# Performance work log

Measured on AMD Instinct MI355X. Metric: run time of the kernel, lower is better.

## Reference

```python
import jax, jax.numpy as jnp
import numpy as np

B, N, DIM, HEADS = 8, 512, 512, 16
MAX_DIST, NG = 128, 32
RBF_STOP = 20.0
EPS = 1e-5


def _ln(x, g, b):
    m = jnp.mean(x, axis=-1, keepdims=True)
    v = jnp.mean((x - m) ** 2, axis=-1, keepdims=True)
    return (x - m) * jax.lax.rsqrt(v + EPS) * g + b


def setup_inputs() -> dict:
    key = jax.random.key(0)
    ks = jax.random.split(key, 12)
    d = DIM
    s = 0.02
    return {
        "x": jax.random.normal(ks[0], (B * N, d), jnp.float32),
        "dist_matrix": jax.random.randint(ks[1], (B, N, N), 0, MAX_DIST, jnp.int32),
        "dist_3d": jax.random.uniform(ks[2], (B, N, N), jnp.float32) * RBF_STOP,
        "norm1_g": jnp.ones((d,), jnp.float32),
        "norm1_b": jnp.zeros((d,), jnp.float32),
        "in_proj_w": jax.random.normal(ks[3], (3 * d, d), jnp.float32) * s,
        "in_proj_b": jnp.zeros((3 * d,), jnp.float32),
        "out_proj_w": jax.random.normal(ks[4], (d, d), jnp.float32) * s,
        "out_proj_b": jnp.zeros((d,), jnp.float32),
        "dist_emb": jax.random.normal(ks[5], (MAX_DIST, HEADS), jnp.float32) * s,
        "rbf_w": jax.random.normal(ks[6], (HEADS, NG), jnp.float32) * s,
        "rbf_b": jnp.zeros((HEADS,), jnp.float32),
        "norm2_g": jnp.ones((d,), jnp.float32),
        "norm2_b": jnp.zeros((d,), jnp.float32),
        "ffn_w1": jax.random.normal(ks[7], (4 * d, d), jnp.float32) * s,
        "ffn_b1": jnp.zeros((4 * d,), jnp.float32),
        "ffn_w2": jax.random.normal(ks[8], (d, 4 * d), jnp.float32) * s,
        "ffn_b2": jnp.zeros((d,), jnp.float32),
        "batch": jnp.repeat(jnp.arange(B, dtype=jnp.int32), N),
    }


def reference(x, dist_matrix, dist_3d, norm1_g, norm1_b, in_proj_w, in_proj_b,
              out_proj_w, out_proj_b, dist_emb, rbf_w, rbf_b, norm2_g, norm2_b,
              ffn_w1, ffn_b1, ffn_w2, ffn_b2, batch):
    b, n = dist_matrix.shape[0], dist_matrix.shape[1]
    d = x.shape[-1]
    dh = d // HEADS
    # equal-size graphs -> to_dense_batch is a reshape, mask all-true
    xd = x.reshape(b, n, d)

    # additive attention bias: shortest-path-distance embedding + RBF projection
    dc = jnp.clip(dist_matrix, 0, MAX_DIST - 1)
    bias_spd = dist_emb[dc]                                  # [b, n, n, H]
    offset = jnp.linspace(0.0, RBF_STOP, NG, dtype=jnp.float32)
    coeff = -0.5 / (RBF_STOP / (NG - 1)) ** 2
    rbf = jnp.exp(coeff * (dist_3d[..., None] - offset) ** 2)  # [b, n, n, NG]
    bias_3d = rbf @ rbf_w.T + rbf_b                          # [b, n, n, H]
    bias = jnp.transpose(bias_spd + bias_3d, (0, 3, 1, 2))   # [b, H, n, n]

    # multi-head attention (pre-norm residual, as in source)
    h = _ln(xd, norm1_g, norm1_b)
    qkv = h @ in_proj_w.T + in_proj_b
    q, k, v = jnp.split(qkv, 3, axis=-1)
    q = q.reshape(b, n, HEADS, dh).transpose(0, 2, 1, 3)
    k = k.reshape(b, n, HEADS, dh).transpose(0, 2, 1, 3)
    v = v.reshape(b, n, HEADS, dh).transpose(0, 2, 1, 3)
    scores = jnp.einsum('bhqd,bhkd->bhqk', q, k) / jnp.sqrt(jnp.float32(dh)) + bias
    attn = jax.nn.softmax(scores, axis=-1)
    ctx = jnp.einsum('bhqk,bhkd->bhqd', attn, v)
    ctx = ctx.transpose(0, 2, 1, 3).reshape(b, n, d)
    attn_out = ctx @ out_proj_w.T + out_proj_b
    h = h + attn_out

    # FFN (dropout inactive at eval)
    h2 = _ln(h, norm2_g, norm2_b)
    ff = jax.nn.gelu(h2 @ ffn_w1.T + ffn_b1, approximate=False) @ ffn_w2.T + ffn_b2
    h = h + ff
    return h.reshape(b * n, d)
```

## Files before the change

### kernel.cpp

```cpp
#include <hip/hip_runtime.h>
#include <hip/hip_bf16.h>
#include <math.h>

#define BB 8
#define NN 512
#define DD 512
#define NH 16
#define DH 32
#define TD 1536
#define NG 32
#define MAXD 128

typedef __attribute__((ext_vector_type(8))) short bf16x8;
typedef __attribute__((ext_vector_type(4))) float f32x4;
typedef __attribute__((ext_vector_type(2))) unsigned int u32x2;
typedef __attribute__((ext_vector_type(4))) unsigned int u32x4;

__device__ inline short f2bf(float x) {
    __hip_bfloat16 h = __float2bfloat16(x);
    return *reinterpret_cast<short*>(&h);
}
__device__ inline float bf2f(short x) {
    union { unsigned u; float f; } c;
    c.u = ((unsigned)(unsigned short)x) << 16;
    return c.f;
}
__device__ inline unsigned cvt_pk_bf16(float lo, float hi) {
    unsigned r;
    asm("v_cvt_pk_bf16_f32 %0, %1, %2" : "=v"(r) : "v"(lo), "v"(hi));
    return r;
}
__device__ inline float exp2fast(float x) {
    float r;
    asm("v_exp_f32 %0, %1" : "=v"(r) : "v"(x));
    return r;
}

__device__ inline void gld_lds16(const void* g, void* l) {
    __builtin_amdgcn_global_load_lds(
        (const __attribute__((address_space(1))) unsigned int*)g,
        (__attribute__((address_space(3))) unsigned int*)l, 16, 0, 0);
}

__global__ __launch_bounds__(256) void cvt_weights(
    const float* __restrict__ s0, const float* __restrict__ s1,
    const float* __restrict__ s2, const float* __restrict__ s3,
    short* __restrict__ d0, short* __restrict__ d1,
    short* __restrict__ d2, short* __restrict__ d3,
    const float* __restrict__ rbfw, const float* __restrict__ rbfb,
    short* __restrict__ Tg,
    int n0, int n1, int n2, int n3) {
    if (blockIdx.y == 4) {
        if (blockIdx.x != 0) return;
        const float STEP  = 20.0f / 31.0f;
        const float COEFF = -0.5f / (STEP * STEP);
        for (int idx = threadIdx.x; idx < 194 * 16; idx += 256) {
            const int i = idx >> 4, h = idx & 15;
            const float x = fminf((float)i, 192.0f) * (20.0f / 192.0f);
            float acc = rbfb[h];
#pragma unroll
            for (int g = 0; g < NG; g++) {
                const float t = x - (float)g * STEP;
                acc += __expf(COEFF * t * t) * rbfw[h * NG + g];
            }
            Tg[idx] = f2bf(acc * 1.44269504088896f);
        }
        return;
    }
    const float* s; short* d; int n;
    switch (blockIdx.y) {
        case 0: s = s0; d = d0; n = n0; break;
        case 1: s = s1; d = d1; n = n1; break;
        case 2: s = s2; d = d2; n = n2; break;
        default: s = s3; d = d3; n = n3; break;
    }
    const int i = (blockIdx.x * 256 + threadIdx.x) * 4;
    if (i >= n) return;
    const float4 v = *(const float4*)(s + i);
    short4 o;
    o.x = f2bf(v.x); o.y = f2bf(v.y); o.z = f2bf(v.z); o.w = f2bf(v.w);
    *(short4*)(d + i) = o;
}

__global__ __launch_bounds__(256) void ln_kernel(const float* __restrict__ x,
                                                 const float* __restrict__ g,
                                                 const float* __restrict__ b,
                                                 short* __restrict__ out_bf) {
    const int row = blockIdx.x;
    const int tid = threadIdx.x;
    const int wave = tid >> 6, lane = tid & 63;
    const float* xr = x + (size_t)row * DD;
    const float v0 = xr[tid], v1 = xr[tid + 256];
    float s = v0 + v1, q = v0 * v0 + v1 * v1;
#pragma unroll
    for (int m = 1; m < 64; m <<= 1) { s += __shfl_xor(s, m); q += __shfl_xor(q, m); }
    __shared__ float ps[8];
    if (lane == 0) { ps[wave] = s; ps[wave + 4] = q; }
    __syncthreads();
    s = ps[0] + ps[1] + ps[2] + ps[3];
    q = ps[4] + ps[5] + ps[6] + ps[7];
    const float mean = s * (1.0f / DD);
    const float var  = q * (1.0f / DD) - mean * mean;
    const float rs   = rsqrtf(var + 1e-5f);
    out_bf[(size_t)row * DD + tid]       = f2bf((v0 - mean) * rs * g[tid] + b[tid]);
    out_bf[(size_t)row * DD + tid + 256] = f2bf((v1 - mean) * rs * g[tid + 256] + b[tid + 256]);
}

template <int TM, bool GELU, int RESMODE, bool OUTBF>
__global__ __launch_bounds__(256) void gemm_bf16(
    const short* __restrict__ A, const short* __restrict__ Bw,
    const float* __restrict__ bias, const void* __restrict__ res,
    void* __restrict__ Cout, int M, int Nout, int K) {
    const int MI = TM / 32;
    const int bm = blockIdx.y * TM;
    const int bn = blockIdx.x * 128;
    const int tid  = threadIdx.x;
    const int wave = tid >> 6;
    const int lane = tid & 63;
    const int l16  = lane & 15;
    const int quad = lane >> 4;
    const int wr = (wave >> 1) * (TM / 2);
    const int wc = (wave & 1) * 64;

    __shared__ short As[2][TM * 32];
    __shared__ short Bs[2][128 * 32];

    f32x4 acc[MI][4];
#pragma unroll
    for (int i = 0; i < MI; i++)
#pragma unroll
        for (int j = 0; j < 4; j++) acc[i][j] = (f32x4){0.f, 0.f, 0.f, 0.f};

    auto stage = [&](int buf, int k0) {
        const short* Ab = A + (size_t)bm * K + k0;
        const short* Bb = Bw + (size_t)bn * K + k0;
#pragma unroll
        for (int j = 0; j < TM / 64; j++) {
            const int idx = j * 256 + wave * 64 + lane;
            gld_lds16(Ab + (size_t)(idx >> 2) * K + (idx & 3) * 8,
                      &As[buf][(size_t)(j * 256 + wave * 64) * 8]);
        }
#pragma unroll
        for (int j = 0; j < 2; j++) {
            const int idx = j * 256 + wave * 64 + lane;
            gld_lds16(Bb + (size_t)(idx >> 2) * K + (idx & 3) * 8,
                      &Bs[buf][(size_t)(j * 256 + wave * 64) * 8]);
        }
    };
    auto compute = [&](int buf) {
        bf16x8 af[MI], bfr[4];
#pragma unroll
        for (int i = 0; i < MI; i++)
            af[i] = *(const bf16x8*)&As[buf][(wr + i * 16 + l16) * 32 + quad * 8];
#pragma unroll
        for (int j = 0; j < 4; j++)
            bfr[j] = *(const bf16x8*)&Bs[buf][(wc + j * 16 + l16) * 32 + quad * 8];
#pragma unroll
        for (int i = 0; i < MI; i++)
#pragma unroll
            for (int j = 0; j < 4; j++)
                acc[i][j] = __builtin_amdgcn_mfma_f32_16x16x32_bf16(af[i], bfr[j], acc[i][j], 0, 0, 0);
    };

    stage(0, 0);
    __syncthreads();
    int cur = 0;
    for (int k0 = 32; k0 < K; k0 += 32) {
        stage(cur ^ 1, k0);
        compute(cur);
        __syncthreads();
        cur ^= 1;
    }
    compute(cur);

#pragma unroll
    for (int i = 0; i < MI; i++) {
#pragma unroll
        for (int r = 0; r < 4; r++) {
            const int row = bm + wr + i * 16 + quad * 4 + r;
#pragma unroll
            for (int j = 0; j < 4; j++) {
                const int col = bn + wc + j * 16 + l16;
                float v = acc[i][j][r] + bias[col];
                if (GELU) v = 0.5f * v * (1.0f + erff(v * 0.70710678118654752f));
                if (RESMODE == 1) v += ((const float*)res)[(size_t)row * Nout + col];
                if (RESMODE == 2) v += bf2f(((const short*)res)[(size_t)row * Nout + col]);
                if (OUTBF) ((short*)Cout)[(size_t)row * Nout + col] = f2bf(v);
                else       ((float*)Cout)[(size_t)row * Nout + col] = v;
            }
        }
    }
}

__global__ __launch_bounds__(512, 2) void attn_mfma(
    const short* __restrict__ qkv,
    const int* __restrict__ dist,
    const float* __restrict__ dist3d,
    const float* __restrict__ demb,
    const short* __restrict__ Tg,
    short* __restrict__ Obf) {
    const int blk  = blockIdx.x;
    const int b    = blk & 7;
    const int q0   = (blk >> 3) * 16;
    const int tid  = threadIdx.x;
    const int wave = tid >> 6;
    const int lane = tid & 63;
    const int l16  = lane & 15;
    const int quad = lane >> 4;
    const int hh0  = wave * 2;

    __shared__ short Vc[2][NH * 1024];
    __shared__ short Pb[16 * 512];
    __shared__ short Tt[194 * 18];
    __shared__ short Db[128 * 18];
    __shared__ unsigned short Pk[512 * 16];

    for (int i = tid; i < 194 * 16; i += 512) Tt[(i >> 4) * 18 + (i & 15)] = Tg[i];
    for (int i = tid; i < 128 * 16; i += 512)
        Db[(i >> 4) * 18 + (i & 15)] = f2bf(demb[i] * 1.44269504088896f);
    {
        const size_t rb = ((size_t)(b * NN) + q0) * NN;
#pragma unroll
        for (int q = 0; q < 16; q++) {
            const size_t off = rb + (size_t)q * NN + tid;
            int dc = dist[off];
            dc = min(max(dc, 0), MAXD - 1);
            int ii = (int)(dist3d[off] * 9.6f + 0.5f);
            ii = min(ii, 192);
            Pk[tid * 16 + q] = (unsigned short)(dc | (ii << 8));
        }
    }

    const float scale = 0.17677669529663687f * 1.44269504088896f;
    bf16x8 qf[2];
#pragma unroll
    for (int h = 0; h < 2; h++)
        qf[h] = *(const bf16x8*)(qkv + (size_t)(b * NN + q0 + l16) * TD + (hh0 + h) * DH + quad * 8);

    f32x4 O[2][2];
    float lsum[2][4];
#pragma unroll
    for (int h = 0; h < 2; h++) {
#pragma unroll
        for (int tt = 0; tt < 2; tt++) O[h][tt] = (f32x4){0.f, 0.f, 0.f, 0.f};
#pragma unroll
        for (int r = 0; r < 4; r++) lsum[h][r] = 0.f;
    }

    __syncthreads();

    const int sk = lane >> 2;
    const int sc = lane & 3;

    auto stageV = [&](int buf, int c) {
        const size_t rowb = (size_t)(b * NN + c * 32 + sk) * TD + 2 * DD + sc * 8;
#pragma unroll
        for (int h = 0; h < 2; h++) {
            short* dst = &Vc[buf][(hh0 + h) * 1024];
            gld_lds16(qkv + rowb + (hh0 + h) * DH, dst);
            gld_lds16(qkv + rowb + (size_t)16 * TD + (hh0 + h) * DH, dst + 512);
        }
    };
    auto loadK = [&](int c, bf16x8 (*kd)[2]) {
#pragma unroll
        for (int h = 0; h < 2; h++) {
            const short* base =
                qkv + (size_t)(b * NN + c * 32 + l16) * TD + DD + (hh0 + h) * DH + quad * 8;
            kd[h][0] = *(const bf16x8*)base;
            kd[h][1] = *(const bf16x8*)(base + 16 * TD);
        }
    };

    bf16x8 kf[2][2], kfn[2][2];
    stageV(0, 0);
    loadK(0, kf);
    int cur = 0;

    for (int c = 0; c < 16; c++) {
        asm volatile("" ::: "memory");
        __builtin_amdgcn_s_waitcnt(0x0F70);
        asm volatile("" ::: "memory");

        u32x2 vraw[2][4];
#pragma unroll
        for (int h = 0; h < 2; h++) {
            const unsigned va =
                (unsigned)(uintptr_t)&Vc[cur][(hh0 + h) * 1024 + quad * 128 + l16];
            asm volatile("ds_read_b64_tr_b16 %0, %1 offset:0"    : "=v"(vraw[h][0]) : "v"(va));
            asm volatile("ds_read_b64_tr_b16 %0, %1 offset:128"  : "=v"(vraw[h][1]) : "v"(va));
            asm volatile("ds_read_b64_tr_b16 %0, %1 offset:1024" : "=v"(vraw[h][2]) : "v"(va));
            asm volatile("ds_read_b64_tr_b16 %0, %1 offset:1152" : "=v"(vraw[h][3]) : "v"(va));
        }

        if (c + 1 < 16) {
            stageV(cur ^ 1, c + 1);
            loadK(c + 1, kfn);
        }

#pragma unroll
        for (int half = 0; half < 2; half++) {
            const ushort4 pk4 =
                *(const ushort4*)&Pk[(unsigned)((c * 32 + half * 16 + l16) * 16 + quad * 4)];
            const unsigned short pe[4] = {pk4.x, pk4.y, pk4.z, pk4.w};
            float bb[2][4];
#pragma unroll
            for (int r = 0; r < 4; r++) {
                const unsigned u  = pe[r];
                const unsigned dc = u & 0xFFu;
                const unsigned ii = u >> 8;
                const unsigned du = *(const unsigned*)&Db[dc * 18 + hh0];
                const unsigned tu = *(const unsigned*)&Tt[ii * 18 + hh0];
                union { unsigned x; float f; } a0, a1, b0, b1;
                a0.x = du << 16; a1.x = du & 0xFFFF0000u;
                b0.x = tu << 16; b1.x = tu & 0xFFFF0000u;
                bb[0][r] = a0.f + b0.f;
                bb[1][r] = a1.f + b1.f;
            }
#pragma unroll
            for (int h = 0; h < 2; h++) {
                f32x4 s = __builtin_amdgcn_mfma_f32_16x16x32_bf16(
                    qf[h], kf[h][half], (f32x4){0.f, 0.f, 0.f, 0.f}, 0, 0, 0);
                float pv[4];
#pragma unroll
                for (int r = 0; r < 4; r++) {
                    float sv = s[r] * scale + bb[h][r];
                    sv = fminf(sv, 28.853901f);
                    pv[r] = exp2fast(sv);
                    lsum[h][r] += pv[r];
                }
                u32x2 w;
                w[0] = cvt_pk_bf16(pv[0], pv[1]);
                w[1] = cvt_pk_bf16(pv[2], pv[3]);
                *(u32x2*)&Pb[(wave * 2 + h) * 512 + (half * 16 + l16) * 16 + quad * 4] = w;
            }
        }

        asm volatile("" ::: "memory");
        asm volatile("s_waitcnt lgkmcnt(0)" ::: "memory");
        __builtin_amdgcn_sched_barrier(0);

        u32x2 praw[2][2];
#pragma unroll
        for (int h = 0; h < 2; h++) {
            const unsigned pa =
                (unsigned)(uintptr_t)&Pb[(wave * 2 + h) * 512 + quad * 64 + l16];
            asm volatile("ds_read_b64_tr_b16 %0, %1 offset:0"   : "=v"(praw[h][0]) : "v"(pa));
            asm volatile("ds_read_b64_tr_b16 %0, %1 offset:512" : "=v"(praw[h][1]) : "v"(pa));
        }
        asm volatile("s_waitcnt lgkmcnt(0)" ::: "memory");
        __builtin_amdgcn_sched_barrier(0);

        __builtin_amdgcn_s_setprio(1);
#pragma unroll
        for (int h = 0; h < 2; h++) {
            union { u32x4 u; bf16x8 s; } pf, v0, v1;
            pf.u = (u32x4){praw[h][0][0], praw[h][0][1], praw[h][1][0], praw[h][1][1]};
#pragma unroll
            for (int r = 0; r < 4; r++) {
                v0.u[r] = __builtin_amdgcn_perm(vraw[h][r][1], vraw[h][r][0], 0x05040100u);
                v1.u[r] = __builtin_amdgcn_perm(vraw[h][r][1], vraw[h][r][0], 0x07060302u);
            }
            O[h][0] = __builtin_amdgcn_mfma_f32_16x16x32_bf16(pf.s, v0.s, O[h][0], 0, 0, 0);
            O[h][1] = __builtin_amdgcn_mfma_f32_16x16x32_bf16(pf.s, v1.s, O[h][1], 0, 0, 0);
        }
        __builtin_amdgcn_s_setprio(0);

#pragma unroll
        for (int h = 0; h < 2; h++) { kf[h][0] = kfn[h][0]; kf[h][1] = kfn[h][1]; }
        cur ^= 1;
    }

#pragma unroll
    for (int h = 0; h < 2; h++) {
        const int hh = hh0 + h;
#pragma unroll
        for (int m = 1; m < 16; m <<= 1)
#pragma unroll
            for (int r = 0; r < 4; r++) lsum[h][r] += __shfl_xor(lsum[h][r], m);
#pragma unroll
        for (int r = 0; r < 4; r++) {
            const float rl = 1.0f / lsum[h][r];
            const size_t row = (size_t)(b * NN + q0 + quad * 4 + r);
#pragma unroll
            for (int tt = 0; tt < 2; tt++)
                Obf[row * DD + hh * DH + tt * 16 + l16] = f2bf(O[h][tt][r] * rl);
        }
    }
}

extern "C" void kernel_launch(void* const* d_in, const int* in_sizes, int n_in,
                              void* d_out, int out_size, void* d_ws, size_t ws_size,
                              hipStream_t stream) {
    const float* x      = (const float*)d_in[0];
    const int*   dist   = (const int*)d_in[1];
    const float* dist3d = (const float*)d_in[2];
    const float* n1g    = (const float*)d_in[3];
    const float* n1b    = (const float*)d_in[4];
    const float* win    = (const float*)d_in[5];
    const float* bin    = (const float*)d_in[6];
    const float* wo     = (const float*)d_in[7];
    const float* bo     = (const float*)d_in[8];
    const float* demb   = (const float*)d_in[9];
    const float* rbfw   = (const float*)d_in[10];
    const float* rbfb   = (const float*)d_in[11];
    const float* n2g    = (const float*)d_in[12];
    const float* n2b    = (const float*)d_in[13];
    const float* w1     = (const float*)d_in[14];
    const float* b1     = (const float*)d_in[15];
    const float* w2     = (const float*)d_in[16];
    const float* b2     = (const float*)d_in[17];

    char* p = (char*)d_ws;
    short* h_bf   = (short*)p; p += (size_t)4096 * 512 * 2;
    short* qkv_bf = (short*)p; p += (size_t)4096 * 1536 * 2;
    float* hres   = (float*)p; p += (size_t)4096 * 512 * 4;
    short* h2_bf  = (short*)p; p += (size_t)4096 * 512 * 2;
    short* win_bf = (short*)p; p += (size_t)1536 * 512 * 2;
    short* wo_bf  = (short*)p; p += (size_t)512 * 512 * 2;
    short* w1_bf  = (short*)p; p += (size_t)2048 * 512 * 2;
    short* w2_bf  = (short*)p; p += (size_t)512 * 2048 * 2;
    short* Tg     = (short*)p; p += (size_t)8192;
    short* o_bf   = (short*)p;
    short* mid_bf = (short*)p;
    p += (size_t)4096 * 2048 * 2;

    const int M = BB * NN;

    cvt_weights<<<dim3(1024, 5), 256, 0, stream>>>(
        win, wo, w1, w2, win_bf, wo_bf, w1_bf, w2_bf, rbfw, rbfb, Tg,
        1536 * 512, 512 * 512, 2048 * 512, 512 * 2048);
    ln_kernel<<<M, 256, 0, stream>>>(x, n1g, n1b, h_bf);
    gemm_bf16<128, false, 0, true><<<dim3(12, 32), 256, 0, stream>>>(
        h_bf, win_bf, bin, nullptr, qkv_bf, M, TD, DD);
    attn_mfma<<<256, 512, 0, stream>>>(
        qkv_bf, dist, dist3d, demb, Tg, o_bf);
    gemm_bf16<64, false, 2, false><<<dim3(4, 64), 256, 0, stream>>>(
        o_bf, wo_bf, bo, h_bf, hres, M, DD, DD);
    ln_kernel<<<M, 256, 0, stream>>>(hres, n2g, n2b, h2_bf);
    gemm_bf16<128, true, 0, true><<<dim3(16, 32), 256, 0, stream>>>(
        h2_bf, w1_bf, b1, nullptr, mid_bf, M, 2048, DD);
    gemm_bf16<64, false, 1, false><<<dim3(4, 64), 256, 0, stream>>>(
        mid_bf, w2_bf, b2, hres, (float*)d_out, M, DD, 2048);
}
```

Measured before the change: 239.4 us.

## Vectorize epilogues and conversions, shrink GEMM M-tiles for more blocks

GEMM operands in the MFMA are swapped so each lane holds four consecutive output columns, which lets the epilogue use vector loads and stores for bias, residual and output. LayerNorm and weight conversion now use wider vector loads and packed bf16 conversion. Small GEMMs (QKV, out-proj, FFN2) get smaller M tiles (64/32) so more blocks fill the CUs. The smaller tiles give less reuse per block, and the TM=32 staging path leaves half the threads idle during A loads.

Result: no change. 241.6 us (+0.9%).

```diff
diff --git a/kernel.cpp b/kernel.cpp
--- a/kernel.cpp
+++ b/kernel.cpp
@@ -74,12 +74,16 @@
         case 2: s = s2; d = d2; n = n2; break;
         default: s = s3; d = d3; n = n3; break;
     }
-    const int i = (blockIdx.x * 256 + threadIdx.x) * 4;
+    const int i = (blockIdx.x * 256 + threadIdx.x) * 8;
     if (i >= n) return;
-    const float4 v = *(const float4*)(s + i);
-    short4 o;
-    o.x = f2bf(v.x); o.y = f2bf(v.y); o.z = f2bf(v.z); o.w = f2bf(v.w);
-    *(short4*)(d + i) = o;
+    const float4 a = *(const float4*)(s + i);
+    const float4 b = *(const float4*)(s + i + 4);
+    u32x4 o;
+    o[0] = cvt_pk_bf16(a.x, a.y);
+    o[1] = cvt_pk_bf16(a.z, a.w);
+    o[2] = cvt_pk_bf16(b.x, b.y);
+    o[3] = cvt_pk_bf16(b.z, b.w);
+    *(u32x4*)(d + i) = o;
 }
 
 __global__ __launch_bounds__(256) void ln_kernel(const float* __restrict__ x,
@@ -90,8 +94,8 @@
     const int tid = threadIdx.x;
     const int wave = tid >> 6, lane = tid & 63;
     const float* xr = x + (size_t)row * DD;
-    const float v0 = xr[tid], v1 = xr[tid + 256];
-    float s = v0 + v1, q = v0 * v0 + v1 * v1;
+    const float2 v01 = *(const float2*)(xr + 2 * tid);
+    float s = v01.x + v01.y, q = v01.x * v01.x + v01.y * v01.y;
 #pragma unroll
     for (int m = 1; m < 64; m <<= 1) { s += __shfl_xor(s, m); q += __shfl_xor(q, m); }
     __shared__ float ps[8];
@@ -102,8 +106,11 @@
     const float mean = s * (1.0f / DD);
     const float var  = q * (1.0f / DD) - mean * mean;
     const float rs   = rsqrtf(var + 1e-5f);
-    out_bf[(size_t)row * DD + tid]       = f2bf((v0 - mean) * rs * g[tid] + b[tid]);
-    out_bf[(size_t)row * DD + tid + 256] = f2bf((v1 - mean) * rs * g[tid + 256] + b[tid + 256]);
+    const float2 g2 = *(const float2*)(g + 2 * tid);
+    const float2 b2 = *(const float2*)(b + 2 * tid);
+    const float o0 = (v01.x - mean) * rs * g2.x + b2.x;
+    const float o1 = (v01.y - mean) * rs * g2.y + b2.y;
+    *(unsigned*)&out_bf[(size_t)row * DD + 2 * tid] = cvt_pk_bf16(o0, o1);
 }
 
 template <int TM, bool GELU, int RESMODE, bool OUTBF>
@@ -111,7 +118,7 @@
     const short* __restrict__ A, const short* __restrict__ Bw,
     const float* __restrict__ bias, const void* __restrict__ res,
     void* __restrict__ Cout, int M, int Nout, int K) {
-    const int MI = TM / 32;
+    const int MI = (TM >= 32) ? TM / 32 : 1;
     const int bm = blockIdx.y * TM;
     const int bn = blockIdx.x * 128;
     const int tid  = threadIdx.x;
@@ -134,15 +141,21 @@
     auto stage = [&](int buf, int k0) {
         const short* Ab = A + (size_t)bm * K + k0;
         const short* Bb = Bw + (size_t)bn * K + k0;
-#pragma unroll
-        for (int j = 0; j < TM / 64; j++) {
-            const int idx = j * 256 + wave * 64 + lane;
-            gld_lds16(Ab + (size_t)(idx >> 2) * K + (idx & 3) * 8,
-                      &As[buf][(size_t)(j * 256 + wave * 64) * 8]);
+        if (TM >= 64) {
+#pragma unroll
+            for (int j = 0; j < TM / 64; j++) {
+                const int idx = j * 256 + tid;
+                gld_lds16(Ab + (size_t)(idx >> 2) * K + (idx & 3) * 8,
+                          &As[buf][(size_t)(j * 256 + wave * 64) * 8]);
+            }
+        } else {
+            if (tid < 128)
+                gld_lds16(Ab + (size_t)(tid >> 2) * K + (tid & 3) * 8,
+                          &As[buf][(size_t)(wave * 64) * 8]);
         }
 #pragma unroll
         for (int j = 0; j < 2; j++) {
-            const int idx = j * 256 + wave * 64 + lane;
+            const int idx = j * 256 + tid;
             gld_lds16(Bb + (size_t)(idx >> 2) * K + (idx & 3) * 8,
                       &Bs[buf][(size_t)(j * 256 + wave * 64) * 8]);
         }
@@ -159,7 +172,7 @@
         for (int i = 0; i < MI; i++)
 #pragma unroll
             for (int j = 0; j < 4; j++)
-                acc[i][j] = __builtin_amdgcn_mfma_f32_16x16x32_bf16(af[i], bfr[j], acc[i][j], 0, 0, 0);
+                acc[i][j] = __builtin_amdgcn_mfma_f32_16x16x32_bf16(bfr[j], af[i], acc[i][j], 0, 0, 0);
     };
 
     stage(0, 0);
@@ -175,18 +188,34 @@
 
 #pragma unroll
     for (int i = 0; i < MI; i++) {
-#pragma unroll
-        for (int r = 0; r < 4; r++) {
-            const int row = bm + wr + i * 16 + quad * 4 + r;
-#pragma unroll
-            for (int j = 0; j < 4; j++) {
-                const int col = bn + wc + j * 16 + l16;
-                float v = acc[i][j][r] + bias[col];
-                if (GELU) v = 0.5f * v * (1.0f + erff(v * 0.70710678118654752f));
-                if (RESMODE == 1) v += ((const float*)res)[(size_t)row * Nout + col];
-                if (RESMODE == 2) v += bf2f(((const short*)res)[(size_t)row * Nout + col]);
-                if (OUTBF) ((short*)Cout)[(size_t)row * Nout + col] = f2bf(v);
-                else       ((float*)Cout)[(size_t)row * Nout + col] = v;
+        const int row = bm + wr + i * 16 + l16;
+#pragma unroll
+        for (int j = 0; j < 4; j++) {
+            const int col = bn + wc + j * 16 + quad * 4;
+            const float4 b4 = *(const float4*)&bias[col];
+            float v[4] = {acc[i][j][0] + b4.x, acc[i][j][1] + b4.y,
+                          acc[i][j][2] + b4.z, acc[i][j][3] + b4.w};
+            if (GELU) {
+#pragma unroll
+                for (int r = 0; r < 4; r++)
+                    v[r] = 0.5f * v[r] * (1.0f + erff(v[r] * 0.70710678118654752f));
+            }
+            if (RESMODE == 1) {
+                const float4 r4 = *(const float4*)&((const float*)res)[(size_t)row * Nout + col];
+                v[0] += r4.x; v[1] += r4.y; v[2] += r4.z; v[3] += r4.w;
+            }
+            if (RESMODE == 2) {
+                const short4 r4 = *(const short4*)&((const short*)res)[(size_t)row * Nout + col];
+                v[0] += bf2f(r4.x); v[1] += bf2f(r4.y); v[2] += bf2f(r4.z); v[3] += bf2f(r4.w);
+            }
+            if (OUTBF) {
+                u32x2 o;
+                o[0] = cvt_pk_bf16(v[0], v[1]);
+                o[1] = cvt_pk_bf16(v[2], v[3]);
+                *(u32x2*)&((short*)Cout)[(size_t)row * Nout + col] = o;
+            } else {
+                *(float4*)&((float*)Cout)[(size_t)row * Nout + col] =
+                    (float4){v[0], v[1], v[2], v[3]};
             }
         }
     }
@@ -426,19 +455,19 @@
 
     const int M = BB * NN;
 
-    cvt_weights<<<dim3(1024, 5), 256, 0, stream>>>(
+    cvt_weights<<<dim3(512, 5), 256, 0, stream>>>(
         win, wo, w1, w2, win_bf, wo_bf, w1_bf, w2_bf, rbfw, rbfb, Tg,
         1536 * 512, 512 * 512, 2048 * 512, 512 * 2048);
     ln_kernel<<<M, 256, 0, stream>>>(x, n1g, n1b, h_bf);
-    gemm_bf16<128, false, 0, true><<<dim3(12, 32), 256, 0, stream>>>(
+    gemm_bf16<64, false, 0, true><<<dim3(12, 64), 256, 0, stream>>>(
         h_bf, win_bf, bin, nullptr, qkv_bf, M, TD, DD);
     attn_mfma<<<256, 512, 0, stream>>>(
         qkv_bf, dist, dist3d, demb, Tg, o_bf);
-    gemm_bf16<64, false, 2, false><<<dim3(4, 64), 256, 0, stream>>>(
+    gemm_bf16<32, false, 2, false><<<dim3(4, 128), 256, 0, stream>>>(
         o_bf, wo_bf, bo, h_bf, hres, M, DD, DD);
     ln_kernel<<<M, 256, 0, stream>>>(hres, n2g, n2b, h2_bf);
     gemm_bf16<128, true, 0, true><<<dim3(16, 32), 256, 0, stream>>>(
         h2_bf, w1_bf, b1, nullptr, mid_bf, M, 2048, DD);
-    gemm_bf16<64, false, 1, false><<<dim3(4, 64), 256, 0, stream>>>(
+    gemm_bf16<32, false, 1, false><<<dim3(4, 128), 256, 0, stream>>>(
         mid_bf, w2_bf, b2, hres, (float*)d_out, M, DD, 2048);
 }
```
